# Performance work log

Measured on AMD Instinct MI355X. Metric: run time of the kernel, lower is better.

Reference implementation:

```python
import jax, jax.numpy as jnp
import numpy as np

H, W = 256, 256
N = 512


def setup_inputs() -> dict:
    key = jax.random.key(0)
    k1, k2, k3, k4, k5 = jax.random.split(key, 5)
    # gaussian centers in front of the camera
    xy = jax.random.normal(k1, (N, 2), dtype=jnp.float32) * 3.0
    z = jax.random.uniform(k2, (N,), dtype=jnp.float32, minval=2.0, maxval=45.0)
    means3D = jnp.concatenate([xy, z[:, None]], axis=1)  # (N,3)
    # SPD 3x3 covariances
    A = jax.random.normal(k3, (N, 3, 3), dtype=jnp.float32) * 0.2
    covs3d = jnp.einsum('nij,nkj->nik', A, A) + 0.05 * jnp.eye(3, dtype=jnp.float32)
    colors = jax.random.uniform(k4, (N, 3), dtype=jnp.float32)
    opacities = jax.random.uniform(k5, (N,), dtype=jnp.float32)
    K = jnp.array([[300.0, 0.0, W / 2.0], [0.0, 300.0, H / 2.0], [0.0, 0.0, 1.0]], dtype=jnp.float32)
    R = jnp.eye(3, dtype=jnp.float32)
    t = jnp.zeros((3,), dtype=jnp.float32)
    return {"means3D": means3D, "covs3d": covs3d, "colors": colors,
            "opacities": opacities, "K": K, "R": R, "t": t}


def _render(means3D, covs3d, colors, opacities, K, R, t):
    # --- projection ---
    cam = means3D @ R.T + t                       # (N,3)
    Z = cam[:, 2]                                 # raw camera-space depth
    depths = jnp.maximum(Z, 1.0)                  # clamped (used for sort/mask)
    screen = cam @ K.T
    means2D = screen[:, :2] / screen[:, 2:3]      # (N,2)
    fx, fy = K[0, 0], K[1, 1]
    zeros = jnp.zeros_like(Z)
    # Jacobian of perspective projection, (N,2,3); uses raw Z as in the original
    J = jnp.stack([
        jnp.stack([fx / Z, zeros, -fx * cam[:, 0] / (Z * Z)], axis=-1),
        jnp.stack([zeros, fy / Z, -fy * cam[:, 1] / (Z * Z)], axis=-1),
    ], axis=1)
    covs_cam = jnp.einsum('ij,njk,lk->nil', R, covs3d, R)     # R Sigma R^T
    covs2D = jnp.einsum('nij,njk,nlk->nil', J, covs_cam, J)   # J Sigma_cam J^T, (N,2,2)

    valid = (depths > 1.0) & (depths < 50.0)
    # front-to-back sort by clamped depth
    idx = jnp.argsort(depths)
    means2D = means2D[idx]
    covs2D = covs2D[idx]
    colors_s = colors[idx]
    op_s = opacities[idx]
    valid = valid[idx]

    # --- per-gaussian per-pixel density ---
    covs2D = covs2D + 1e-4 * jnp.eye(2, dtype=covs2D.dtype)
    cov_inv = jnp.linalg.inv(covs2D)              # (N,2,2)
    cov_det = jnp.linalg.det(covs2D)              # (N,)
    norm = 1.0 / (2.0 * jnp.pi * jnp.sqrt(cov_det))

    ys, xs = jnp.meshgrid(jnp.arange(H, dtype=jnp.float32),
                          jnp.arange(W, dtype=jnp.float32), indexing='ij')
    pixels = jnp.stack([xs, ys], axis=-1)         # (H,W,2), [x,y]

    dx = pixels[None] - means2D[:, None, None, :]                 # (N,H,W,2)
    expo = -0.5 * jnp.einsum('nhwi,nij,nhwj->nhw', dx, cov_inv, dx)
    gaussian = norm[:, None, None] * jnp.exp(expo)                # (N,H,W)
    gaussian = gaussian * valid.astype(gaussian.dtype)[:, None, None]

    # --- alpha compositing (inclusive cumprod as in the original) ---
    alphas = op_s[:, None, None] * gaussian                       # (N,H,W)
    T = jnp.cumprod(1.0 - alphas, axis=0)
    weights = alphas * T
    rendered = jnp.einsum('nhw,nc->hwc', weights, colors_s)       # (H,W,3)
    return rendered


def reference(means3D, covs3d, colors, opacities, K, R, t):
    return _render(means3D, covs3d, colors, opacities, K, R, t)
```

## Files before the change

kernel.cpp:

```cpp
#include <hip/hip_runtime.h>


constexpr int   REC   = 16;
constexpr int   WIMG  = 256;
constexpr int   HIMG  = 256;
constexpr int   SPLIT = 8;
constexpr float LOG2E  = 1.4426950408889634f;
constexpr float INV2PI = 0.15915494309189535f;
constexpr float TWOLN2 = 1.3862943611198906f;
constexpr float LOG2EPS = -29.897352853986263f;

__global__ __launch_bounds__(512) void gs_preprocess(
    const float* __restrict__ means3D, const float* __restrict__ covs3d,
    const float* __restrict__ colors,  const float* __restrict__ opac,
    const float* __restrict__ Km,      const float* __restrict__ Rm,
    const float* __restrict__ tvec,    float* __restrict__ recs, int N)
{
    __shared__ float s_depth[512];
    __shared__ int   s_cnt[64][9];
    const int t  = threadIdx.x;
    const int l  = t & 63, p = t >> 6;
    const int gi = (int)blockIdx.x * 64 + l;

    float d_all = 3.0e38f;
    if (t < N) {
        const float m0 = means3D[t*3+0], m1 = means3D[t*3+1], m2 = means3D[t*3+2];
        d_all = fmaxf(Rm[6]*m0 + Rm[7]*m1 + Rm[8]*m2 + tvec[2], 1.0f);
    }
    s_depth[t] = d_all;
    __syncthreads();

    const float dg = s_depth[gi & 511];
    int cnt = 0;
    #pragma unroll 16
    for (int j = p*64; j < p*64 + 64; ++j) {
        const float dj = s_depth[j];
        cnt += (dj < dg) || (dj == dg && j < gi);
    }
    s_cnt[l][p] = cnt;

    float rec[13];
    const bool act = (p == 0) && (gi < N);
    if (act) {
        float Kl[9], Rl[9], tl[3];
        #pragma unroll
        for (int k = 0; k < 9; ++k) { Kl[k] = Km[k]; Rl[k] = Rm[k]; }
        tl[0] = tvec[0]; tl[1] = tvec[1]; tl[2] = tvec[2];

        const float m0 = means3D[gi*3+0], m1 = means3D[gi*3+1], m2 = means3D[gi*3+2];
        const float cam0 = Rl[0]*m0 + Rl[1]*m1 + Rl[2]*m2 + tl[0];
        const float cam1 = Rl[3]*m0 + Rl[4]*m1 + Rl[5]*m2 + tl[1];
        const float cam2 = Rl[6]*m0 + Rl[7]*m1 + Rl[8]*m2 + tl[2];
        const float Z = cam2;
        const float depth = fmaxf(Z, 1.0f);

        const float s0 = Kl[0]*cam0 + Kl[1]*cam1 + Kl[2]*cam2;
        const float s1 = Kl[3]*cam0 + Kl[4]*cam1 + Kl[5]*cam2;
        const float s2 = Kl[6]*cam0 + Kl[7]*cam1 + Kl[8]*cam2;
        const float mx = s0 / s2, my = s1 / s2;

        const float fx = Kl[0], fy = Kl[4];
        const float iz = 1.0f / Z;
        float J[2][3];
        J[0][0] = fx*iz; J[0][1] = 0.0f;  J[0][2] = -fx*cam0*iz*iz;
        J[1][0] = 0.0f;  J[1][1] = fy*iz; J[1][2] = -fy*cam1*iz*iz;

        float S[9];
        #pragma unroll
        for (int k = 0; k < 9; ++k) S[k] = covs3d[gi*9+k];

        float RS[9], Cc[9];
        #pragma unroll
        for (int r = 0; r < 3; ++r)
            #pragma unroll
            for (int c = 0; c < 3; ++c)
                RS[r*3+c] = Rl[r*3+0]*S[0+c] + Rl[r*3+1]*S[3+c] + Rl[r*3+2]*S[6+c];
        #pragma unroll
        for (int r = 0; r < 3; ++r)
            #pragma unroll
            for (int c = 0; c < 3; ++c)
                Cc[r*3+c] = RS[r*3+0]*Rl[c*3+0] + RS[r*3+1]*Rl[c*3+1] + RS[r*3+2]*Rl[c*3+2];

        float JC[2][3];
        #pragma unroll
        for (int r = 0; r < 2; ++r)
            #pragma unroll
            for (int c = 0; c < 3; ++c)
                JC[r][c] = J[r][0]*Cc[0+c] + J[r][1]*Cc[3+c] + J[r][2]*Cc[6+c];

        const float c200 = JC[0][0]*J[0][0] + JC[0][1]*J[0][1] + JC[0][2]*J[0][2] + 1e-4f;
        const float c201 = JC[0][0]*J[1][0] + JC[0][1]*J[1][1] + JC[0][2]*J[1][2];
        const float c210 = JC[1][0]*J[0][0] + JC[1][1]*J[0][1] + JC[1][2]*J[0][2];
        const float c211 = JC[1][0]*J[1][0] + JC[1][1]*J[1][1] + JC[1][2]*J[1][2] + 1e-4f;

        const float det  = c200*c211 - c201*c210;
        const float idet = 1.0f / det;
        const float ia  = c211*idet;
        const float ibs = -(c201 + c210)*idet;
        const float ic  = c200*idet;

        const bool  valid = (depth > 1.0f) && (depth < 50.0f);
        const float nrm   = valid ? (INV2PI / sqrtf(det)) : 0.0f;
        const float opn   = opac[gi] * nrm;

        float x0, x1, y0, y1;
        if (opn > 1e-9f) {
            const float q0 = log2f(opn) - LOG2EPS;
            const float s  = TWOLN2 * q0;
            const float bx = sqrtf(s * c200);
            const float by = sqrtf(s * c211);
            x0 = mx - bx; x1 = mx + bx;
            y0 = my - by; y1 = my + by;
        } else {
            x0 = 1e30f; x1 = -1e30f; y0 = 1e30f; y1 = -1e30f;
        }

        rec[0]  = x0; rec[1] = x1; rec[2] = y0; rec[3] = y1;
        rec[4]  = mx; rec[5] = my;
        rec[6]  = -0.5f*LOG2E*ia;
        rec[7]  = -0.5f*LOG2E*ibs;
        rec[8]  = -0.5f*LOG2E*ic;
        rec[9]  = opn;
        rec[10] = colors[gi*3+0];
        rec[11] = colors[gi*3+1];
        rec[12] = colors[gi*3+2];
    }
    __syncthreads();

    if (act) {
        int rank = 0;
        #pragma unroll
        for (int q = 0; q < 8; ++q) rank += s_cnt[l][q];
        float4* dst = (float4*)(recs + rank*REC);
        dst[0] = make_float4(rec[0],  rec[1],  rec[2],  rec[3]);
        dst[1] = make_float4(rec[4],  rec[5],  rec[6],  rec[7]);
        dst[2] = make_float4(rec[8],  rec[9],  rec[10], rec[11]);
        dst[3] = make_float4(rec[12], 0.0f,    0.0f,    0.0f);
    }
}

__global__ __launch_bounds__(512, 8) void gs_render(
    const float* __restrict__ recs, float* __restrict__ out, int N)
{
    __shared__ float  s_bb0[512], s_bb1[512], s_bb2[512], s_bb3[512];
    __shared__ float  s_ev[512][12];
    __shared__ float4 s_part[SPLIT][64];

    const int t = threadIdx.x;

    if (t < N) {
        const float4 a = *(const float4*)(recs + t*REC + 0);
        const float4 b = *(const float4*)(recs + t*REC + 4);
        const float4 c = *(const float4*)(recs + t*REC + 8);
        const float4 d = *(const float4*)(recs + t*REC + 12);
        s_bb0[t] = a.x; s_bb1[t] = a.y; s_bb2[t] = a.z; s_bb3[t] = a.w;
        s_ev[t][0] = b.x; s_ev[t][1] = b.y; s_ev[t][2] = b.z; s_ev[t][3] = b.w;
        s_ev[t][4] = c.x; s_ev[t][5] = c.y; s_ev[t][6] = c.z; s_ev[t][7] = c.w;
        s_ev[t][8] = d.x;
    } else {
        s_bb0[t] = 1e30f; s_bb1[t] = -1e30f; s_bb2[t] = 1e30f; s_bb3[t] = -1e30f;
    }
    __syncthreads();

    const int w    = t >> 6;
    const int lane = t & 63;
    const float sx0 = (float)(((int)blockIdx.x & 3) * 64);
    const float sx1 = sx0 + 63.0f;
    const float px  = sx0 + (float)lane;
    const float py  = (float)((int)blockIdx.x >> 2);

    const int base = w * 64;
    bool hit;
    {
        const float x0 = s_bb0[base+lane], x1 = s_bb1[base+lane];
        const float y0 = s_bb2[base+lane], y1 = s_bb3[base+lane];
        hit = !(x1 < sx0 || x0 > sx1 || y1 < py || y0 > py);
    }
    unsigned long long mask = __ballot(hit);

    float T = 1.0f, cr = 0.0f, cg = 0.0f, cb = 0.0f;
    while (mask) {
        const int k = __builtin_ctzll(mask);
        mask &= mask - 1;
        const float* e = s_ev[base + k];
        const float dx = px - e[0];
        const float dy = py - e[1];
        const float e2 = fmaf(e[2], dx*dx, fmaf(e[3], dx*dy, e[4]*dy*dy));
        const float al = e[5] * __builtin_amdgcn_exp2f(e2);
        T *= (1.0f - al);
        const float wt = al * T;
        cr = fmaf(wt, e[6], cr);
        cg = fmaf(wt, e[7], cg);
        cb = fmaf(wt, e[8], cb);
    }

    s_part[w][lane] = make_float4(T, cr, cg, cb);
    __syncthreads();

    if (t < 64) {
        float4 f = s_part[0][t];
        float Ta = f.x, r_ = f.y, g_ = f.z, b_ = f.w;
        #pragma unroll
        for (int k = 1; k < SPLIT; ++k) {
            const float4 p = s_part[k][t];
            r_ = fmaf(Ta, p.y, r_);
            g_ = fmaf(Ta, p.z, g_);
            b_ = fmaf(Ta, p.w, b_);
            Ta *= p.x;
        }
        const int o = ((int)blockIdx.x * 64 + t) * 3;
        out[o+0] = r_;
        out[o+1] = g_;
        out[o+2] = b_;
    }
}

extern "C" void kernel_launch(void* const* d_in, const int* in_sizes, int n_in,
                              void* d_out, int out_size, void* d_ws, size_t ws_size,
                              hipStream_t stream)
{
    const float* means3D = (const float*)d_in[0];
    const float* covs3d  = (const float*)d_in[1];
    const float* colors  = (const float*)d_in[2];
    const float* opac    = (const float*)d_in[3];
    const float* Km      = (const float*)d_in[4];
    const float* Rm      = (const float*)d_in[5];
    const float* tv      = (const float*)d_in[6];
    const int N = in_sizes[3];

    float* recs = (float*)d_ws;
    float* out  = (float*)d_out;

    gs_preprocess<<<dim3((N + 63) / 64), dim3(512), 0, stream>>>(
        means3D, covs3d, colors, opac, Km, Rm, tv, recs, N);

    gs_render<<<dim3(WIMG * HIMG / 64), dim3(512), 0, stream>>>(recs, out, N);
}
```

Baseline: 17.47 us.

## Use exact ellipse-vs-row-segment culling, vectorize LDS reads, coalesce output stores

Replaces the axis-aligned bounding-box cull with an exact test: each Gaussian's 2D ellipse is intersected with the 64-pixel row segment, using per-Gaussian conditional parameters (c1, c2) and a log threshold computed in preprocessing. The aim is to reject more Gaussians before the per-pixel composite loop. The per-Gaussian evaluation record is repacked so the render loop reads it with two float4 LDS loads, and output RGB is staged through shared memory so stores are coalesced. The cull costs a few more FLOPs per candidate and adds an extra barrier for the output write.

```diff
diff --git a/kernel.cpp b/kernel.cpp
--- a/kernel.cpp
+++ b/kernel.cpp
@@ -7,8 +7,7 @@
 constexpr int   SPLIT = 8;
 constexpr float LOG2E  = 1.4426950408889634f;
 constexpr float INV2PI = 0.15915494309189535f;
-constexpr float TWOLN2 = 1.3862943611198906f;
-constexpr float LOG2EPS = -29.897352853986263f;
+constexpr float INVEPS = 1.0e7f;
 
 __global__ __launch_bounds__(512) void gs_preprocess(
     const float* __restrict__ means3D, const float* __restrict__ covs3d,
@@ -95,28 +94,21 @@
 
         const float det  = c200*c211 - c201*c210;
         const float idet = 1.0f / det;
-        const float ia  = c211*idet;
-        const float ibs = -(c201 + c210)*idet;
-        const float ic  = c200*idet;
+        const float ia   = c211*idet;
+        const float i01  = -0.5f*(c201 + c210)*idet;
+        const float ic   = c200*idet;
+        const float ibs  = 2.0f*i01;
 
         const bool  valid = (depth > 1.0f) && (depth < 50.0f);
         const float nrm   = valid ? (INV2PI / sqrtf(det)) : 0.0f;
         const float opn   = opac[gi] * nrm;
 
-        float x0, x1, y0, y1;
-        if (opn > 1e-9f) {
-            const float q0 = log2f(opn) - LOG2EPS;
-            const float s  = TWOLN2 * q0;
-            const float bx = sqrtf(s * c200);
-            const float by = sqrtf(s * c211);
-            x0 = mx - bx; x1 = mx + bx;
-            y0 = my - by; y1 = my + by;
-        } else {
-            x0 = 1e30f; x1 = -1e30f; y0 = 1e30f; y1 = -1e30f;
-        }
-
-        rec[0]  = x0; rec[1] = x1; rec[2] = y0; rec[3] = y1;
-        rec[4]  = mx; rec[5] = my;
+        const float c1 = i01 / ia;
+        const float c2 = ic - i01*i01/ia;
+        const float L2 = 2.0f * logf(opn * INVEPS);
+
+        rec[0]  = my;  rec[1] = c2;  rec[2] = L2;  rec[3] = c1;
+        rec[4]  = mx;  rec[5] = ia;
         rec[6]  = -0.5f*LOG2E*ia;
         rec[7]  = -0.5f*LOG2E*ibs;
         rec[8]  = -0.5f*LOG2E*ic;
@@ -142,9 +134,10 @@
 __global__ __launch_bounds__(512, 8) void gs_render(
     const float* __restrict__ recs, float* __restrict__ out, int N)
 {
-    __shared__ float  s_bb0[512], s_bb1[512], s_bb2[512], s_bb3[512];
+    __shared__ float  s_my[512], s_c2[512], s_L2[512], s_c1[512], s_mx[512], s_p0[512];
     __shared__ float  s_ev[512][12];
     __shared__ float4 s_part[SPLIT][64];
+    __shared__ float  s_rgb[192];
 
     const int t = threadIdx.x;
 
@@ -153,28 +146,34 @@
         const float4 b = *(const float4*)(recs + t*REC + 4);
         const float4 c = *(const float4*)(recs + t*REC + 8);
         const float4 d = *(const float4*)(recs + t*REC + 12);
-        s_bb0[t] = a.x; s_bb1[t] = a.y; s_bb2[t] = a.z; s_bb3[t] = a.w;
-        s_ev[t][0] = b.x; s_ev[t][1] = b.y; s_ev[t][2] = b.z; s_ev[t][3] = b.w;
-        s_ev[t][4] = c.x; s_ev[t][5] = c.y; s_ev[t][6] = c.z; s_ev[t][7] = c.w;
+        s_my[t] = a.x; s_c2[t] = a.y; s_L2[t] = a.z; s_c1[t] = a.w;
+        s_mx[t] = b.x; s_p0[t] = b.y;
+        float4* ev = (float4*)s_ev[t];
+        ev[0] = make_float4(b.x, a.x, b.z, b.w);
+        ev[1] = make_float4(c.x, c.y, c.z, c.w);
         s_ev[t][8] = d.x;
     } else {
-        s_bb0[t] = 1e30f; s_bb1[t] = -1e30f; s_bb2[t] = 1e30f; s_bb3[t] = -1e30f;
+        s_my[t] = 0.0f; s_c2[t] = 0.0f; s_L2[t] = -1e30f;
+        s_c1[t] = 0.0f; s_mx[t] = 0.0f; s_p0[t] = 1.0f;
     }
     __syncthreads();
 
     const int w    = t >> 6;
     const int lane = t & 63;
     const float sx0 = (float)(((int)blockIdx.x & 3) * 64);
-    const float sx1 = sx0 + 63.0f;
+    const float scx = sx0 + 31.5f;
     const float px  = sx0 + (float)lane;
     const float py  = (float)((int)blockIdx.x >> 2);
 
     const int base = w * 64;
     bool hit;
     {
-        const float x0 = s_bb0[base+lane], x1 = s_bb1[base+lane];
-        const float y0 = s_bb2[base+lane], y1 = s_bb3[base+lane];
-        hit = !(x1 < sx0 || x0 > sx1 || y1 < py || y0 > py);
+        const int j = base + lane;
+        const float dy  = py - s_my[j];
+        const float rem = fmaf(-s_c2[j], dy*dy, s_L2[j]);
+        const float xc  = fmaf(-s_c1[j], dy, s_mx[j]);
+        const float t1  = fmaxf(fabsf(xc - scx) - 31.5f, 0.0f);
+        hit = (s_p0[j]*t1*t1 <= rem);
     }
     unsigned long long mask = __ballot(hit);
 
@@ -183,15 +182,18 @@
         const int k = __builtin_ctzll(mask);
         mask &= mask - 1;
         const float* e = s_ev[base + k];
-        const float dx = px - e[0];
-        const float dy = py - e[1];
-        const float e2 = fmaf(e[2], dx*dx, fmaf(e[3], dx*dy, e[4]*dy*dy));
-        const float al = e[5] * __builtin_amdgcn_exp2f(e2);
+        const float4 v0 = *(const float4*)(e + 0);
+        const float4 v1 = *(const float4*)(e + 4);
+        const float  bl = e[8];
+        const float dx = px - v0.x;
+        const float dy = py - v0.y;
+        const float e2 = fmaf(v0.z, dx*dx, fmaf(v0.w, dx*dy, v1.x*dy*dy));
+        const float al = v1.y * __builtin_amdgcn_exp2f(e2);
         T *= (1.0f - al);
         const float wt = al * T;
-        cr = fmaf(wt, e[6], cr);
-        cg = fmaf(wt, e[7], cg);
-        cb = fmaf(wt, e[8], cb);
+        cr = fmaf(wt, v1.z, cr);
+        cg = fmaf(wt, v1.w, cg);
+        cb = fmaf(wt, bl,  cb);
     }
 
     s_part[w][lane] = make_float4(T, cr, cg, cb);
@@ -208,10 +210,14 @@
             b_ = fmaf(Ta, p.w, b_);
             Ta *= p.x;
         }
-        const int o = ((int)blockIdx.x * 64 + t) * 3;
-        out[o+0] = r_;
-        out[o+1] = g_;
-        out[o+2] = b_;
+        s_rgb[t*3+0] = r_;
+        s_rgb[t*3+1] = g_;
+        s_rgb[t*3+2] = b_;
+    }
+    __syncthreads();
+
+    if (t < 192) {
+        out[(int)blockIdx.x * 192 + t] = s_rgb[t];
     }
 }
 
```

Result: faster. 16.11 us (-7.8%).
